# Optimization experiments

Measured on AMD Instinct MI355X. Metric: run time of the kernel, lower is better.

Reference implementation:

```python
import jax, jax.numpy as jnp
import numpy as np

B = 384          # batch; must equal F for the final broadcast to be valid
F = 384          # out_features
H = 64           # hidden_dim
TAU = 1.0        # d_k passed to attention()
EPS = 1e-12      # F.normalize eps


def _l2_normalize(x):
    # torch F.normalize(p=2, dim=-1): x / max(||x||, eps)
    n = jnp.sqrt(jnp.sum(x * x, axis=-1, keepdims=True))
    return x / jnp.maximum(n, EPS)


def setup_inputs() -> dict:
    key = jax.random.key(0)
    kx, kwq, kbq, kwk, kbk = jax.random.split(key, 5)
    bound = 1.0 / np.sqrt(F)  # torch Linear default init range
    x = jax.random.normal(kx, (B, F), dtype=jnp.float32)
    Wq = jax.random.uniform(kwq, (F * H, F), jnp.float32, -bound, bound)
    bq = jax.random.uniform(kbq, (F * H,), jnp.float32, -bound, bound)
    Wk = jax.random.uniform(kwk, (F * H, F), jnp.float32, -bound, bound)
    bk = jax.random.uniform(kbk, (F * H,), jnp.float32, -bound, bound)
    return {"x": x, "Wq": Wq, "bq": bq, "Wk": Wk, "bk": bk}


def reference(x, Wq, bq, Wk, bk):
    # q = qs(x), k = ks(x): [B, F*H] -> reshape [B, F, H]
    q = (x @ Wq.T + bq).reshape(B, F, H)
    k = (x @ Wk.T + bk).reshape(B, F, H)
    # L2-normalized QK attention with temperature sqrt(tau)
    q = _l2_normalize(q)
    k = _l2_normalize(k)
    scores = jnp.einsum('bfh,bgh->bfg', q, k) / jnp.sqrt(jnp.float32(TAU))
    scores = jax.nn.softmax(scores, axis=-1)  # [B, F, F]
    # faithful to `input * scores`: x[B,F] left-pads to [1,B,F]; valid since B==F
    return x * scores
```

## Files before the change

### kernel.cpp

```cpp
#include <hip/hip_runtime.h>
#include <hip/hip_bf16.h>


typedef __attribute__((ext_vector_type(8))) short bf16x8;
typedef __attribute__((ext_vector_type(4))) float f32x4;

__device__ __forceinline__ ushort f2bf(float f) {
  union { __hip_bfloat16 h; ushort u; } c;
  c.h = __float2bfloat16(f);
  return c.u;
}

__global__ __launch_bounds__(256) void qk_gemm(
    const float* __restrict__ xin,
    const float* __restrict__ Wq, const float* __restrict__ bq,
    const float* __restrict__ Wk, const float* __restrict__ bk,
    ushort* __restrict__ qhat, ushort* __restrict__ khat)
{
  const int n0 = blockIdx.x * 64;
  const float* W    = blockIdx.y ? Wk : Wq;
  const float* bias = blockIdx.y ? bk : bq;
  ushort* outp      = blockIdx.y ? khat : qhat;

  __shared__ __align__(16) ushort Alds[384 * 40];
  __shared__ __align__(16) ushort Blds[64 * 40];

  const int tid  = threadIdx.x;
  const int wave = tid >> 6;
  const int lane = tid & 63;
  const int l15  = lane & 15;
  const int lhi  = lane >> 4;

  f32x4 acc[6][4];
  #pragma unroll
  for (int m = 0; m < 6; ++m)
    #pragma unroll
    for (int n = 0; n < 4; ++n) acc[m][n] = (f32x4)(0.f);

  for (int k0 = 0; k0 < 384; k0 += 32) {
    #pragma unroll
    for (int i = 0; i < 12; ++i) {
      int idx = tid + 256 * i;
      int row = idx >> 3, c4 = idx & 7;
      float4 v = *reinterpret_cast<const float4*>(xin + row * 384 + k0 + c4 * 4);
      ushort4 u = make_ushort4(f2bf(v.x), f2bf(v.y), f2bf(v.z), f2bf(v.w));
      *reinterpret_cast<ushort4*>(&Alds[row * 40 + c4 * 4]) = u;
    }
    #pragma unroll
    for (int i = 0; i < 2; ++i) {
      int idx = tid + 256 * i;
      int row = idx >> 3, c4 = idx & 7;
      float4 v = *reinterpret_cast<const float4*>(W + (size_t)(n0 + row) * 384 + k0 + c4 * 4);
      ushort4 u = make_ushort4(f2bf(v.x), f2bf(v.y), f2bf(v.z), f2bf(v.w));
      *reinterpret_cast<ushort4*>(&Blds[row * 40 + c4 * 4]) = u;
    }
    __syncthreads();

    bf16x8 bfr[4];
    #pragma unroll
    for (int nf = 0; nf < 4; ++nf)
      bfr[nf] = *reinterpret_cast<const bf16x8*>(&Blds[(nf * 16 + l15) * 40 + lhi * 8]);
    #pragma unroll
    for (int mf = 0; mf < 6; ++mf) {
      bf16x8 afr = *reinterpret_cast<const bf16x8*>(
          &Alds[(wave * 96 + mf * 16 + l15) * 40 + lhi * 8]);
      #pragma unroll
      for (int nf = 0; nf < 4; ++nf)
        acc[mf][nf] = __builtin_amdgcn_mfma_f32_16x16x32_bf16(afr, bfr[nf], acc[mf][nf], 0, 0, 0);
    }
    __syncthreads();
  }

  float bv[4];
  #pragma unroll
  for (int nf = 0; nf < 4; ++nf) bv[nf] = bias[n0 + nf * 16 + l15];

  #pragma unroll
  for (int mf = 0; mf < 6; ++mf) {
    float ss[4];
    #pragma unroll
    for (int j = 0; j < 4; ++j) {
      float s = 0.f;
      #pragma unroll
      for (int nf = 0; nf < 4; ++nf) {
        float v = acc[mf][nf][j] + bv[nf];
        acc[mf][nf][j] = v;
        s += v * v;
      }
      ss[j] = s;
    }
    #pragma unroll
    for (int m = 1; m < 16; m <<= 1) {
      #pragma unroll
      for (int j = 0; j < 4; ++j) ss[j] += __shfl_xor(ss[j], m, 64);
    }
    #pragma unroll
    for (int j = 0; j < 4; ++j) {
      float scale = 1.f / fmaxf(sqrtf(ss[j]), 1e-12f);
      int row = wave * 96 + mf * 16 + lhi * 4 + j;
      #pragma unroll
      for (int nf = 0; nf < 4; ++nf)
        outp[(size_t)row * 24576 + n0 + nf * 16 + l15] = f2bf(acc[mf][nf][j] * scale);
    }
  }
}

__global__ __launch_bounds__(256) void attn_out(
    const float* __restrict__ xin,
    const ushort* __restrict__ qhat,
    const ushort* __restrict__ khat,
    float* __restrict__ out)
{
  const int f0 = blockIdx.x * 32;
  const int b  = blockIdx.y;

  __shared__ __align__(16) char smem[384 * 72 * 2];
  ushort* Klds = reinterpret_cast<ushort*>(smem);
  float*  Slds = reinterpret_cast<float*>(smem);
  __shared__ __align__(16) ushort Qlds[32 * 72];
  __shared__ float redmax[128], redsum[128], mfin[32], invs[32];

  const int tid  = threadIdx.x;
  const int wave = tid >> 6;
  const int lane = tid & 63;
  const int l15  = lane & 15;
  const int lhi  = lane >> 4;

  #pragma unroll
  for (int i = 0; i < 12; ++i) {
    int idx = tid + 256 * i;
    int row = idx >> 3, c8 = idx & 7;
    uint4 v = *reinterpret_cast<const uint4*>(khat + (size_t)b * 24576 + row * 64 + c8 * 8);
    *reinterpret_cast<uint4*>(&Klds[row * 72 + c8 * 8]) = v;
  }
  {
    int row = tid >> 3, c8 = tid & 7;
    uint4 v = *reinterpret_cast<const uint4*>(qhat + (size_t)b * 24576 + (f0 + row) * 64 + c8 * 8);
    *reinterpret_cast<uint4*>(&Qlds[row * 72 + c8 * 8]) = v;
  }
  __syncthreads();

  f32x4 acc[2][6];
  #pragma unroll
  for (int m = 0; m < 2; ++m)
    #pragma unroll
    for (int n = 0; n < 6; ++n) acc[m][n] = (f32x4)(0.f);

  #pragma unroll
  for (int ks = 0; ks < 2; ++ks) {
    bf16x8 aq[2];
    #pragma unroll
    for (int mf = 0; mf < 2; ++mf)
      aq[mf] = *reinterpret_cast<const bf16x8*>(&Qlds[(mf * 16 + l15) * 72 + ks * 32 + lhi * 8]);
    #pragma unroll
    for (int nf = 0; nf < 6; ++nf) {
      bf16x8 bk8 = *reinterpret_cast<const bf16x8*>(
          &Klds[(wave * 96 + nf * 16 + l15) * 72 + ks * 32 + lhi * 8]);
      #pragma unroll
      for (int mf = 0; mf < 2; ++mf)
        acc[mf][nf] = __builtin_amdgcn_mfma_f32_16x16x32_bf16(aq[mf], bk8, acc[mf][nf], 0, 0, 0);
    }
  }

  #pragma unroll
  for (int mf = 0; mf < 2; ++mf) {
    #pragma unroll
    for (int j = 0; j < 4; ++j) {
      float m = acc[mf][0][j];
      #pragma unroll
      for (int nf = 1; nf < 6; ++nf) m = fmaxf(m, acc[mf][nf][j]);
      #pragma unroll
      for (int s = 1; s < 16; s <<= 1) m = fmaxf(m, __shfl_xor(m, s, 64));
      if (l15 == 0) redmax[wave * 32 + mf * 16 + lhi * 4 + j] = m;
    }
  }
  __syncthreads();
  if (tid < 32)
    mfin[tid] = fmaxf(fmaxf(redmax[tid], redmax[32 + tid]),
                      fmaxf(redmax[64 + tid], redmax[96 + tid]));
  __syncthreads();

  #pragma unroll
  for (int mf = 0; mf < 2; ++mf) {
    #pragma unroll
    for (int j = 0; j < 4; ++j) {
      int r = mf * 16 + lhi * 4 + j;
      float m = mfin[r];
      float s = 0.f;
      #pragma unroll
      for (int nf = 0; nf < 6; ++nf) {
        float p = __expf(acc[mf][nf][j] - m);
        Slds[r * 392 + wave * 96 + nf * 16 + l15] = p;
        s += p;
      }
      #pragma unroll
      for (int sh = 1; sh < 16; sh <<= 1) s += __shfl_xor(s, sh, 64);
      if (l15 == 0) redsum[wave * 32 + r] = s;
    }
  }
  __syncthreads();
  if (tid < 32)
    invs[tid] = 1.f / (redsum[tid] + redsum[32 + tid] + redsum[64 + tid] + redsum[96 + tid]);
  __syncthreads();

  #pragma unroll
  for (int i = 0; i < 12; ++i) {
    int idx = tid + 256 * i;
    int row = idx / 96, c = idx - row * 96;
    float iv = invs[row];
    float4 p4 = *reinterpret_cast<const float4*>(&Slds[row * 392 + c * 4]);
    float4 x4 = *reinterpret_cast<const float4*>(xin + (size_t)(f0 + row) * 384 + c * 4);
    float4 o;
    o.x = x4.x * p4.x * iv;  o.y = x4.y * p4.y * iv;
    o.z = x4.z * p4.z * iv;  o.w = x4.w * p4.w * iv;
    *reinterpret_cast<float4*>(out + (size_t)b * 147456 + (size_t)(f0 + row) * 384 + c * 4) = o;
  }
}

extern "C" void kernel_launch(void* const* d_in, const int* in_sizes, int n_in,
                              void* d_out, int out_size, void* d_ws, size_t ws_size,
                              hipStream_t stream) {
  const float* x  = (const float*)d_in[0];
  const float* Wq = (const float*)d_in[1];
  const float* bq = (const float*)d_in[2];
  const float* Wk = (const float*)d_in[3];
  const float* bk = (const float*)d_in[4];
  float* out = (float*)d_out;

  ushort* qhat = (ushort*)d_ws;
  ushort* khat = qhat + (size_t)384 * 24576;

  dim3 g1(384, 2), b1(256);
  qk_gemm<<<g1, b1, 0, stream>>>(x, Wq, bq, Wk, bk, qhat, khat);

  dim3 g2(12, 384), b2(256);
  attn_out<<<g2, b2, 0, stream>>>(x, qhat, khat, out);
}
```

Before: 137.0 us.

## Pre-convert x to swizzled bf16 and stage tiles with direct global-to-LDS loads

Adds a small pre-pass that converts x to bf16 once, stored in a tile-major XOR-swizzled layout. The GEMM then fills its A tile with global_load_lds instead of re-reading and re-converting fp32 x in every block. The q/k outputs are written with a per-block XOR swizzle so that the attention kernel can load K directly into LDS without padding and read Q fragments straight from global memory, dropping the Q LDS stage. This removes redundant conversion work and LDS bank conflicts, at the cost of an extra kernel launch and some workspace.

Result: faster. 126.5 us (-7.7%).

```diff
diff --git a/kernel.cpp b/kernel.cpp
--- a/kernel.cpp
+++ b/kernel.cpp
@@ -11,18 +11,43 @@
   return c.u;
 }
 
+__device__ __forceinline__ void load_lds16(const void* g, void* l) {
+  __builtin_amdgcn_global_load_lds(
+      (const __attribute__((address_space(1))) void*)g,
+      (__attribute__((address_space(3))) void*)l, 16, 0, 0);
+}
+
+__global__ __launch_bounds__(256) void xconv(const float* __restrict__ xin,
+                                             ushort* __restrict__ xbf) {
+  int t = blockIdx.x * 256 + threadIdx.x;
+  int o = t * 8;
+  int kt = o / 12288;
+  int rem = o - kt * 12288;
+  int m = rem >> 5;
+  int sp = (rem >> 3) & 3;
+  int slot = sp ^ ((m >> 1) & 3);
+  const float* src = xin + m * 384 + kt * 32 + slot * 8;
+  float4 a = *reinterpret_cast<const float4*>(src);
+  float4 b = *reinterpret_cast<const float4*>(src + 4);
+  ushort4 u0 = make_ushort4(f2bf(a.x), f2bf(a.y), f2bf(a.z), f2bf(a.w));
+  ushort4 u1 = make_ushort4(f2bf(b.x), f2bf(b.y), f2bf(b.z), f2bf(b.w));
+  *reinterpret_cast<ushort4*>(xbf + o)     = u0;
+  *reinterpret_cast<ushort4*>(xbf + o + 4) = u1;
+}
+
 __global__ __launch_bounds__(256) void qk_gemm(
-    const float* __restrict__ xin,
+    const ushort* __restrict__ xbf,
     const float* __restrict__ Wq, const float* __restrict__ bq,
     const float* __restrict__ Wk, const float* __restrict__ bk,
     ushort* __restrict__ qhat, ushort* __restrict__ khat)
 {
-  const int n0 = blockIdx.x * 64;
+  const int bx = blockIdx.x;
+  const int n0 = bx * 64;
   const float* W    = blockIdx.y ? Wk : Wq;
   const float* bias = blockIdx.y ? bk : bq;
   ushort* outp      = blockIdx.y ? khat : qhat;
 
-  __shared__ __align__(16) ushort Alds[384 * 40];
+  __shared__ __align__(16) ushort Alds[384 * 32];
   __shared__ __align__(16) ushort Blds[64 * 40];
 
   const int tid  = threadIdx.x;
@@ -37,20 +62,21 @@
     #pragma unroll
     for (int n = 0; n < 4; ++n) acc[m][n] = (f32x4)(0.f);
 
-  for (int k0 = 0; k0 < 384; k0 += 32) {
-    #pragma unroll
-    for (int i = 0; i < 12; ++i) {
-      int idx = tid + 256 * i;
-      int row = idx >> 3, c4 = idx & 7;
-      float4 v = *reinterpret_cast<const float4*>(xin + row * 384 + k0 + c4 * 4);
-      ushort4 u = make_ushort4(f2bf(v.x), f2bf(v.y), f2bf(v.z), f2bf(v.w));
-      *reinterpret_cast<ushort4*>(&Alds[row * 40 + c4 * 4]) = u;
+  const int aslot = lhi ^ ((l15 >> 1) & 3);
+
+  for (int kt = 0; kt < 12; ++kt) {
+    const ushort* asrc = xbf + kt * 12288 + lane * 8;
+    #pragma unroll
+    for (int i = 0; i < 6; ++i) {
+      int chunk = wave * 6 + i;
+      load_lds16(asrc + chunk * 512, (char*)Alds + chunk * 1024);
     }
     #pragma unroll
     for (int i = 0; i < 2; ++i) {
       int idx = tid + 256 * i;
       int row = idx >> 3, c4 = idx & 7;
-      float4 v = *reinterpret_cast<const float4*>(W + (size_t)(n0 + row) * 384 + k0 + c4 * 4);
+      float4 v = *reinterpret_cast<const float4*>(
+          W + (size_t)(n0 + row) * 384 + kt * 32 + c4 * 4);
       ushort4 u = make_ushort4(f2bf(v.x), f2bf(v.y), f2bf(v.z), f2bf(v.w));
       *reinterpret_cast<ushort4*>(&Blds[row * 40 + c4 * 4]) = u;
     }
@@ -62,8 +88,8 @@
       bfr[nf] = *reinterpret_cast<const bf16x8*>(&Blds[(nf * 16 + l15) * 40 + lhi * 8]);
     #pragma unroll
     for (int mf = 0; mf < 6; ++mf) {
-      bf16x8 afr = *reinterpret_cast<const bf16x8*>(
-          &Alds[(wave * 96 + mf * 16 + l15) * 40 + lhi * 8]);
+      int rr = wave * 96 + mf * 16 + l15;
+      bf16x8 afr = *reinterpret_cast<const bf16x8*>(&Alds[rr * 32 + aslot * 8]);
       #pragma unroll
       for (int nf = 0; nf < 4; ++nf)
         acc[mf][nf] = __builtin_amdgcn_mfma_f32_16x16x32_bf16(afr, bfr[nf], acc[mf][nf], 0, 0, 0);
@@ -72,8 +98,13 @@
   }
 
   float bv[4];
-  #pragma unroll
-  for (int nf = 0; nf < 4; ++nf) bv[nf] = bias[n0 + nf * 16 + l15];
+  int hp[4];
+  const int sw = bx & 7;
+  #pragma unroll
+  for (int nf = 0; nf < 4; ++nf) {
+    bv[nf] = bias[n0 + nf * 16 + l15];
+    hp[nf] = (((nf * 2 + (l15 >> 3)) ^ sw) << 3) + (l15 & 7);
+  }
 
   #pragma unroll
   for (int mf = 0; mf < 6; ++mf) {
@@ -100,11 +131,12 @@
       int row = wave * 96 + mf * 16 + lhi * 4 + j;
       #pragma unroll
       for (int nf = 0; nf < 4; ++nf)
-        outp[(size_t)row * 24576 + n0 + nf * 16 + l15] = f2bf(acc[mf][nf][j] * scale);
-    }
-  }
-}
-
+        outp[(size_t)row * 24576 + n0 + hp[nf]] = f2bf(acc[mf][nf][j] * scale);
+    }
+  }
+}
+
+#define PSTR 396
 __global__ __launch_bounds__(256) void attn_out(
     const float* __restrict__ xin,
     const ushort* __restrict__ qhat,
@@ -114,10 +146,9 @@
   const int f0 = blockIdx.x * 32;
   const int b  = blockIdx.y;
 
-  __shared__ __align__(16) char smem[384 * 72 * 2];
+  __shared__ __align__(16) char smem[32 * PSTR * 4];
   ushort* Klds = reinterpret_cast<ushort*>(smem);
   float*  Slds = reinterpret_cast<float*>(smem);
-  __shared__ __align__(16) ushort Qlds[32 * 72];
   __shared__ float redmax[128], redsum[128], mfin[32], invs[32];
 
   const int tid  = threadIdx.x;
@@ -126,18 +157,21 @@
   const int l15  = lane & 15;
   const int lhi  = lane >> 4;
 
+  const ushort* ksrc = khat + (size_t)b * 24576 + lane * 8;
   #pragma unroll
   for (int i = 0; i < 12; ++i) {
-    int idx = tid + 256 * i;
-    int row = idx >> 3, c8 = idx & 7;
-    uint4 v = *reinterpret_cast<const uint4*>(khat + (size_t)b * 24576 + row * 64 + c8 * 8);
-    *reinterpret_cast<uint4*>(&Klds[row * 72 + c8 * 8]) = v;
-  }
-  {
-    int row = tid >> 3, c8 = tid & 7;
-    uint4 v = *reinterpret_cast<const uint4*>(qhat + (size_t)b * 24576 + (f0 + row) * 64 + c8 * 8);
-    *reinterpret_cast<uint4*>(&Qlds[row * 72 + c8 * 8]) = v;
-  }
+    int chunk = wave * 12 + i;
+    load_lds16(ksrc + chunk * 512, smem + chunk * 1024);
+  }
+
+  bf16x8 aq[2][2];
+  #pragma unroll
+  for (int mf = 0; mf < 2; ++mf)
+    #pragma unroll
+    for (int ks = 0; ks < 2; ++ks)
+      aq[mf][ks] = *reinterpret_cast<const bf16x8*>(
+          qhat + (size_t)b * 24576 + (f0 + mf * 16 + l15) * 64 +
+          (((ks * 4 + lhi) ^ (l15 & 7)) << 3));
   __syncthreads();
 
   f32x4 acc[2][6];
@@ -148,17 +182,14 @@
 
   #pragma unroll
   for (int ks = 0; ks < 2; ++ks) {
-    bf16x8 aq[2];
-    #pragma unroll
-    for (int mf = 0; mf < 2; ++mf)
-      aq[mf] = *reinterpret_cast<const bf16x8*>(&Qlds[(mf * 16 + l15) * 72 + ks * 32 + lhi * 8]);
     #pragma unroll
     for (int nf = 0; nf < 6; ++nf) {
+      int rr = wave * 96 + nf * 16 + l15;
       bf16x8 bk8 = *reinterpret_cast<const bf16x8*>(
-          &Klds[(wave * 96 + nf * 16 + l15) * 72 + ks * 32 + lhi * 8]);
+          &Klds[rr * 64 + (((ks * 4 + lhi) ^ (l15 & 7)) << 3)]);
       #pragma unroll
       for (int mf = 0; mf < 2; ++mf)
-        acc[mf][nf] = __builtin_amdgcn_mfma_f32_16x16x32_bf16(aq[mf], bk8, acc[mf][nf], 0, 0, 0);
+        acc[mf][nf] = __builtin_amdgcn_mfma_f32_16x16x32_bf16(aq[mf][ks], bk8, acc[mf][nf], 0, 0, 0);
     }
   }
 
@@ -190,7 +221,7 @@
       #pragma unroll
       for (int nf = 0; nf < 6; ++nf) {
         float p = __expf(acc[mf][nf][j] - m);
-        Slds[r * 392 + wave * 96 + nf * 16 + l15] = p;
+        Slds[r * PSTR + wave * 96 + nf * 16 + l15] = p;
         s += p;
       }
       #pragma unroll
@@ -208,7 +239,7 @@
     int idx = tid + 256 * i;
     int row = idx / 96, c = idx - row * 96;
     float iv = invs[row];
-    float4 p4 = *reinterpret_cast<const float4*>(&Slds[row * 392 + c * 4]);
+    float4 p4 = *reinterpret_cast<const float4*>(&Slds[row * PSTR + c * 4]);
     float4 x4 = *reinterpret_cast<const float4*>(xin + (size_t)(f0 + row) * 384 + c * 4);
     float4 o;
     o.x = x4.x * p4.x * iv;  o.y = x4.y * p4.y * iv;
@@ -229,9 +260,12 @@
 
   ushort* qhat = (ushort*)d_ws;
   ushort* khat = qhat + (size_t)384 * 24576;
+  ushort* xbf  = khat + (size_t)384 * 24576;
+
+  xconv<<<dim3(72), dim3(256), 0, stream>>>(x, xbf);
 
   dim3 g1(384, 2), b1(256);
-  qk_gemm<<<g1, b1, 0, stream>>>(x, Wq, bq, Wk, bk, qhat, khat);
+  qk_gemm<<<g1, b1, 0, stream>>>(xbf, Wq, bq, Wk, bk, qhat, khat);
 
   dim3 g2(12, 384), b2(256);
   attn_out<<<g2, b2, 0, stream>>>(x, qhat, khat, out);
```
